# Kernel optimization log

Measured on AMD Instinct MI355X. Metric: run time of the kernel, lower is better.

The kernel has to match this reference:

```python
import jax, jax.numpy as jnp
import numpy as np

N_NODES = 100000
N_EDGES = 1600000
IN_FEATS = 64
HIDDEN = 64
N_CLASSES = 1


def setup_inputs() -> dict:
    key = jax.random.key(0)
    k0, k1, k2, k3, k4 = jax.random.split(key, 5)
    x = jax.random.normal(k0, (N_NODES, IN_FEATS), dtype=jnp.float32)
    src = jax.random.randint(k1, (N_EDGES,), 0, N_NODES, dtype=jnp.int32)
    dst = jax.random.randint(k2, (N_EDGES,), 0, N_NODES, dtype=jnp.int32)
    W1 = jax.random.normal(k3, (IN_FEATS, HIDDEN), dtype=jnp.float32) * (1.0 / np.sqrt(IN_FEATS))
    b1 = jnp.zeros((HIDDEN,), dtype=jnp.float32)
    W2 = jax.random.normal(k4, (HIDDEN, N_CLASSES), dtype=jnp.float32) * (1.0 / np.sqrt(HIDDEN))
    b2 = jnp.zeros((N_CLASSES,), dtype=jnp.float32)
    return {"x": x, "src": src, "dst": dst, "W1": W1, "b1": b1, "W2": W2, "b2": b2}


def _graph_conv(h, src, dst, W, b, n_nodes):
    # DGL GraphConv, norm='both': D_out^{-1/2} A D_in^{-1/2} h W + b
    ones = jnp.ones(src.shape[0], dtype=h.dtype)
    deg_out = jax.ops.segment_sum(ones, src, num_segments=n_nodes)
    deg_in = jax.ops.segment_sum(ones, dst, num_segments=n_nodes)
    norm_out = jnp.where(deg_out > 0, deg_out, 1.0) ** -0.5  # [N]
    norm_in = jnp.where(deg_in > 0, deg_in, 1.0) ** -0.5
    h = h * norm_out[:, None]
    # project first when it shrinks the message size (matches DGL's in>out path; math identical)
    if W.shape[1] < W.shape[0]:
        h = h @ W
    agg = jax.ops.segment_sum(h[src], dst, num_segments=n_nodes)  # [N, d]
    agg = agg * norm_in[:, None]
    if W.shape[1] >= W.shape[0]:
        agg = agg @ W
    return agg + b


def reference(x, src, dst, W1, b1, W2, b2):
    h = _graph_conv(x, src, dst, W1, b1, N_NODES)
    h = jax.nn.relu(h)
    # dropout p=0.0 -> identity
    h = _graph_conv(h, src, dst, W2, b2, N_NODES)
    return jax.nn.sigmoid(h)
```

## Files before the change

### kernel.cpp

```cpp
#include <hip/hip_runtime.h>

#define NN 100000
#define NE 1600000
#define NW 25000
#define NW4 6250
#define S  64
#define EPS (NE / S)

typedef unsigned int uint;
typedef _Float16 f16x8 __attribute__((ext_vector_type(8)));
typedef _Float16 f16x2 __attribute__((ext_vector_type(2)));
typedef float f32x4 __attribute__((ext_vector_type(4)));

__global__ void __launch_bounds__(256)
k_hist(const int* __restrict__ src, const int* __restrict__ dst,
       uint* __restrict__ partial_in, uint* __restrict__ partial_out,
       unsigned char* __restrict__ lr) {
    __shared__ uint4 cnt4[NW4];
    uint* cnt = (uint*)cnt4;
    int sl = blockIdx.x;
    int y  = blockIdx.y;
    for (int w = threadIdx.x; w < NW4; w += 256) cnt4[w] = make_uint4(0, 0, 0, 0);
    __syncthreads();
    const int* key = y ? src : dst;
    int base = sl * EPS;
    for (int i4 = threadIdx.x; i4 < EPS / 4; i4 += 256) {
        int e = base + i4 * 4;
        int4 k4 = *(const int4*)&key[e];
        uint sh0 = (uint)(k4.x & 3) * 8u, sh1 = (uint)(k4.y & 3) * 8u;
        uint sh2 = (uint)(k4.z & 3) * 8u, sh3 = (uint)(k4.w & 3) * 8u;
        uint r0 = (atomicAdd(&cnt[k4.x >> 2], 1u << sh0) >> sh0) & 0xffu;
        uint r1 = (atomicAdd(&cnt[k4.y >> 2], 1u << sh1) >> sh1) & 0xffu;
        uint r2 = (atomicAdd(&cnt[k4.z >> 2], 1u << sh2) >> sh2) & 0xffu;
        uint r3 = (atomicAdd(&cnt[k4.w >> 2], 1u << sh3) >> sh3) & 0xffu;
        if (y == 0) {
            uchar4 pk = make_uchar4((unsigned char)r0, (unsigned char)r1,
                                    (unsigned char)r2, (unsigned char)r3);
            *(uchar4*)&lr[e] = pk;
        }
    }
    __syncthreads();
    uint4* dp = (uint4*)((y ? partial_out : partial_in) + (size_t)sl * NW);
    for (int w = threadIdx.x; w < NW4; w += 256) dp[w] = cnt4[w];
}

__global__ void k_degnorm(uint* __restrict__ partial_in, const uint* __restrict__ partial_out,
                          int* __restrict__ deg_in, float* __restrict__ norm_in,
                          float* __restrict__ norm_out) {
    int w = blockIdx.x * blockDim.x + threadIdx.x;
    if (w >= NW) return;
    uint run = 0;
#pragma unroll 8
    for (int s = 0; s < S; ++s) {
        uint u = partial_in[(size_t)s * NW + w];
        partial_in[(size_t)s * NW + w] = run;
        run += u;
    }
    uint ro = 0;
#pragma unroll 8
    for (int s = 0; s < S; ++s) ro += partial_out[(size_t)s * NW + w];
    int4 dg;
    float4 fi, fo;
    {
        int d0 = run & 0xff, d1 = (run >> 8) & 0xff, d2 = (run >> 16) & 0xff, d3 = (run >> 24) & 0xff;
        dg = make_int4(d0, d1, d2, d3);
        fi.x = d0 > 0 ? rsqrtf((float)d0) : 1.0f;
        fi.y = d1 > 0 ? rsqrtf((float)d1) : 1.0f;
        fi.z = d2 > 0 ? rsqrtf((float)d2) : 1.0f;
        fi.w = d3 > 0 ? rsqrtf((float)d3) : 1.0f;
        int o0 = ro & 0xff, o1 = (ro >> 8) & 0xff, o2 = (ro >> 16) & 0xff, o3 = (ro >> 24) & 0xff;
        fo.x = o0 > 0 ? rsqrtf((float)o0) : 1.0f;
        fo.y = o1 > 0 ? rsqrtf((float)o1) : 1.0f;
        fo.z = o2 > 0 ? rsqrtf((float)o2) : 1.0f;
        fo.w = o3 > 0 ? rsqrtf((float)o3) : 1.0f;
    }
    *(int4*)&deg_in[w * 4]     = dg;
    *(float4*)&norm_in[w * 4]  = fi;
    *(float4*)&norm_out[w * 4] = fo;
}


__global__ void k_bsum(const int* __restrict__ deg_in, int* __restrict__ bsum) {
    __shared__ int red[4];
    int base = blockIdx.x * 1024;
    int s = 0;
    for (int i = threadIdx.x; i < 1024; i += 256) {
        int n = base + i;
        s += (n < NN) ? deg_in[n] : 0;
    }
#pragma unroll
    for (int off = 32; off; off >>= 1) s += __shfl_xor(s, off, 64);
    if ((threadIdx.x & 63) == 0) red[threadIdx.x >> 6] = s;
    __syncthreads();
    if (threadIdx.x == 0) bsum[blockIdx.x] = red[0] + red[1] + red[2] + red[3];
}

__global__ void k_bscan(const int* __restrict__ bsum, int* __restrict__ bofs,
                        int* __restrict__ row_ofs, int nb) {
    if (blockIdx.x == 0 && threadIdx.x == 0) {
        int run = 0;
        for (int i = 0; i < nb; ++i) { bofs[i] = run; run += bsum[i]; }
        bofs[nb] = run;
        row_ofs[NN] = run;
    }
}

__global__ void k_scan(const int* __restrict__ deg_in, const int* __restrict__ bofs,
                       int* __restrict__ row_ofs) {
    __shared__ int wofs[4];
    int t = threadIdx.x;
    int base = blockIdx.x * 1024 + t * 4;
    int d[4];
#pragma unroll
    for (int k = 0; k < 4; ++k) {
        int n = base + k;
        d[k] = (n < NN) ? deg_in[n] : 0;
    }
    int loc = d[0] + d[1] + d[2] + d[3];
    int v = loc;
    int lane = t & 63;
#pragma unroll
    for (int off = 1; off < 64; off <<= 1) {
        int u = __shfl_up(v, off, 64);
        if (lane >= off) v += u;
    }
    if (lane == 63) wofs[t >> 6] = v;
    __syncthreads();
    int w = t >> 6;
    int wbase = 0;
    if (w > 0) wbase += wofs[0];
    if (w > 1) wbase += wofs[1];
    if (w > 2) wbase += wofs[2];
    int excl = bofs[blockIdx.x] + wbase + (v - loc);
#pragma unroll
    for (int k = 0; k < 4; ++k) {
        int n = base + k;
        if (n < NN) { row_ofs[n] = excl; excl += d[k]; }
    }
}

__global__ void k_replay(const int* __restrict__ src, const int* __restrict__ dst,
                         const uint* __restrict__ base_bytes, const unsigned char* __restrict__ lr,
                         const int* __restrict__ row_ofs, int* __restrict__ csr_src) {
    int e = blockIdx.x * blockDim.x + threadIdx.x;
    if (e < NE) {
        int d  = dst[e];
        int sl = e / EPS;
        uint pw = base_bytes[(size_t)sl * NW + (d >> 2)];
        int b = (int)((pw >> ((d & 3) * 8)) & 0xffu);
        csr_src[row_ofs[d] + b + (int)lr[e]] = src[e];
    }
}

__global__ void __launch_bounds__(256)
k_proj(const float* __restrict__ x, const float* __restrict__ norm_out,
       const float* __restrict__ W1, _Float16* __restrict__ y) {
    int lane = threadIdx.x & 63;
    int col  = lane & 15;
    int kh   = lane >> 4;
    f16x8 wf[4][2];
#pragma unroll
    for (int t = 0; t < 4; ++t)
#pragma unroll
        for (int s = 0; s < 2; ++s)
#pragma unroll
            for (int j = 0; j < 8; ++j)
                wf[t][s][j] = (_Float16)W1[(s * 32 + kh * 8 + j) * 64 + t * 16 + col];
    int tile = blockIdx.x * 4 + (threadIdx.x >> 6);
    if (tile >= NN / 16) return;
    int base = tile * 16;
    int row  = base + col;
    float no = norm_out[row];
    const float* xr = &x[(size_t)row * 64 + kh * 8];
    f16x8 af[2];
#pragma unroll
    for (int s = 0; s < 2; ++s) {
        float4 v0 = *(const float4*)&xr[s * 32];
        float4 v1 = *(const float4*)&xr[s * 32 + 4];
        af[s][0] = (_Float16)(v0.x * no); af[s][1] = (_Float16)(v0.y * no);
        af[s][2] = (_Float16)(v0.z * no); af[s][3] = (_Float16)(v0.w * no);
        af[s][4] = (_Float16)(v1.x * no); af[s][5] = (_Float16)(v1.y * no);
        af[s][6] = (_Float16)(v1.z * no); af[s][7] = (_Float16)(v1.w * no);
    }
    f32x4 acc[4];
#pragma unroll
    for (int t = 0; t < 4; ++t) acc[t] = (f32x4){0.f, 0.f, 0.f, 0.f};
#pragma unroll
    for (int t = 0; t < 4; ++t) {
        acc[t] = __builtin_amdgcn_mfma_f32_16x16x32_f16(af[0], wf[t][0], acc[t], 0, 0, 0);
        acc[t] = __builtin_amdgcn_mfma_f32_16x16x32_f16(af[1], wf[t][1], acc[t], 0, 0, 0);
    }
#pragma unroll
    for (int t = 0; t < 4; ++t)
#pragma unroll
        for (int r = 0; r < 4; ++r)
            y[(size_t)(base + kh * 4 + r) * 64 + t * 16 + col] = (_Float16)acc[t][r];
}

__device__ inline float2 up2(uint u) {
    f16x2 p = __builtin_bit_cast(f16x2, u);
    return make_float2((float)p.x, (float)p.y);
}

__global__ void __launch_bounds__(256)
k_agg1(const int* __restrict__ csr_src, const int* __restrict__ row_ofs,
       const uint* __restrict__ xb, const float* __restrict__ norm_in,
       const float* __restrict__ norm_out,
       const float* __restrict__ b1, const float* __restrict__ W2,
       float* __restrict__ z) {
    int tid = threadIdx.x;
    int lane = tid & 63, q = lane >> 4, lq = lane & 15;
    int n = blockIdx.x * 4 + (tid >> 6);
    if (n >= NN) return;
    int beg = row_ofs[n], end = row_ofs[n + 1];
    float a0 = 0, a1 = 0, a2 = 0, a3 = 0;
    int ei = beg + q;
    for (; ei + 4 < end; ei += 8) {
        int sA = csr_src[ei], sB = csr_src[ei + 4];
        uint2 uA = *(const uint2*)((const char*)xb + ((size_t)sA << 7) + (lq << 3));
        uint2 uB = *(const uint2*)((const char*)xb + ((size_t)sB << 7) + (lq << 3));
        float2 pA0 = up2(uA.x), pA1 = up2(uA.y), pB0 = up2(uB.x), pB1 = up2(uB.y);
        a0 += pA0.x + pB0.x;
        a1 += pA0.y + pB0.y;
        a2 += pA1.x + pB1.x;
        a3 += pA1.y + pB1.y;
    }
    if (ei < end) {
        int sA = csr_src[ei];
        uint2 uA = *(const uint2*)((const char*)xb + ((size_t)sA << 7) + (lq << 3));
        float2 pA0 = up2(uA.x), pA1 = up2(uA.y);
        a0 += pA0.x; a1 += pA0.y; a2 += pA1.x; a3 += pA1.y;
    }
    a0 += __shfl_xor(a0, 16, 64); a0 += __shfl_xor(a0, 32, 64);
    a1 += __shfl_xor(a1, 16, 64); a1 += __shfl_xor(a1, 32, 64);
    a2 += __shfl_xor(a2, 16, 64); a2 += __shfl_xor(a2, 32, 64);
    a3 += __shfl_xor(a3, 16, 64); a3 += __shfl_xor(a3, 32, 64);
    float4 bb = *(const float4*)&b1[lq * 4];
    float4 ww = *(const float4*)&W2[lq * 4];
    float nin = norm_in[n];
    float h0 = fmaxf(a0 * nin + bb.x, 0.0f);
    float h1 = fmaxf(a1 * nin + bb.y, 0.0f);
    float h2 = fmaxf(a2 * nin + bb.z, 0.0f);
    float h3 = fmaxf(a3 * nin + bb.w, 0.0f);
    float zv = h0 * ww.x + h1 * ww.y + h2 * ww.z + h3 * ww.w;
#pragma unroll
    for (int off = 8; off; off >>= 1) zv += __shfl_xor(zv, off, 64);
    if (lane == 0) z[n] = zv * norm_out[n];
}

__global__ void k_out2(const int* __restrict__ csr_src, const int* __restrict__ row_ofs,
                       const float* __restrict__ z, const float* __restrict__ norm_in,
                       const float* __restrict__ b2, float* __restrict__ out) {
    int n = blockIdx.x * blockDim.x + threadIdx.x;
    if (n < NN) {
        int beg = row_ofs[n], end = row_ofs[n + 1];
        float a = 0.0f;
        int i = beg;
        for (; i + 3 < end; i += 4) {
            float z0 = z[csr_src[i]], z1 = z[csr_src[i + 1]];
            float z2 = z[csr_src[i + 2]], z3 = z[csr_src[i + 3]];
            a += (z0 + z1) + (z2 + z3);
        }
        for (; i < end; ++i) a += z[csr_src[i]];
        float v = a * norm_in[n] + b2[0];
        out[n] = 1.0f / (1.0f + expf(-v));
    }
}


extern "C" void kernel_launch(void* const* d_in, const int* in_sizes, int n_in,
                              void* d_out, int out_size, void* d_ws, size_t ws_size,
                              hipStream_t stream) {
    const float* x   = (const float*)d_in[0];
    const int*   src = (const int*)d_in[1];
    const int*   dst = (const int*)d_in[2];
    const float* W1  = (const float*)d_in[3];
    const float* b1  = (const float*)d_in[4];
    const float* W2  = (const float*)d_in[5];
    const float* b2  = (const float*)d_in[6];
    float* out = (float*)d_out;

    uint* W0 = (uint*)d_ws;
    uint*          partial_in  = W0;
    unsigned char* lr          = (unsigned char*)(W0 + 1600000);
    uint*          partial_out = W0 + 2000000;
    uint*          xb          = W0;
    int*           csr_src     = (int*)(W0 + 3600000);
    int*           row_ofs     = (int*)(W0 + 5200000);
    int*           deg_in      = row_ofs + NN + 32;
    float*         norm_in     = (float*)(deg_in + NN);
    float*         norm_out    = norm_in + NN;
    float*         z           = norm_out + NN;
    int*           bsum        = (int*)(z + NN);
    int*           bofs        = bsum + 128;

    int nb = (NN + 1023) / 1024;

    k_hist   <<<dim3(S, 2), 256, 0, stream>>>(src, dst, partial_in, partial_out, lr);
    k_degnorm<<<(NW + 255) / 256, 256, 0, stream>>>(partial_in, partial_out,
                                                    deg_in, norm_in, norm_out);
    k_bsum   <<<nb, 256, 0, stream>>>(deg_in, bsum);
    k_bscan  <<<1, 64, 0, stream>>>(bsum, bofs, row_ofs, nb);
    k_scan   <<<nb, 256, 0, stream>>>(deg_in, bofs, row_ofs);
    k_replay <<<(NE + 255) / 256, 256, 0, stream>>>(src, dst, partial_in, lr, row_ofs, csr_src);

    k_proj   <<<(NN / 16 + 3) / 4, 256, 0, stream>>>(x, norm_out, W1, (_Float16*)xb);
    k_agg1   <<<(NN + 3) / 4, 256, 0, stream>>>(csr_src, row_ofs, xb, norm_in, norm_out,
                                                b1, W2, z);
    k_out2   <<<(NN + 255) / 256, 256, 0, stream>>>(csr_src, row_ofs, z, norm_in, b2, out);
}
```

Baseline: 142.2 us.

## Fuse block sums into degnorm, warp-parallel bscan, persistent unrolled agg1

```diff
diff --git a/kernel.cpp b/kernel.cpp
--- a/kernel.cpp
+++ b/kernel.cpp
@@ -6,6 +6,7 @@
 #define NW4 6250
 #define S  64
 #define EPS (NE / S)
+#define AGG_GRID 2048
 
 typedef unsigned int uint;
 typedef _Float16 f16x8 __attribute__((ext_vector_type(8)));
@@ -46,22 +47,23 @@
 
 __global__ void k_degnorm(uint* __restrict__ partial_in, const uint* __restrict__ partial_out,
                           int* __restrict__ deg_in, float* __restrict__ norm_in,
-                          float* __restrict__ norm_out) {
-    int w = blockIdx.x * blockDim.x + threadIdx.x;
-    if (w >= NW) return;
-    uint run = 0;
+                          float* __restrict__ norm_out, int* __restrict__ bsum) {
+    __shared__ int red[4];
+    int w = blockIdx.x * 256 + threadIdx.x;
+    int mysum = 0;
+    if (w < NW) {
+        uint run = 0;
 #pragma unroll 8
-    for (int s = 0; s < S; ++s) {
-        uint u = partial_in[(size_t)s * NW + w];
-        partial_in[(size_t)s * NW + w] = run;
-        run += u;
-    }
-    uint ro = 0;
+        for (int s = 0; s < S; ++s) {
+            uint u = partial_in[(size_t)s * NW + w];
+            partial_in[(size_t)s * NW + w] = run;
+            run += u;
+        }
+        uint ro = 0;
 #pragma unroll 8
-    for (int s = 0; s < S; ++s) ro += partial_out[(size_t)s * NW + w];
-    int4 dg;
-    float4 fi, fo;
-    {
+        for (int s = 0; s < S; ++s) ro += partial_out[(size_t)s * NW + w];
+        int4 dg;
+        float4 fi, fo;
         int d0 = run & 0xff, d1 = (run >> 8) & 0xff, d2 = (run >> 16) & 0xff, d3 = (run >> 24) & 0xff;
         dg = make_int4(d0, d1, d2, d3);
         fi.x = d0 > 0 ? rsqrtf((float)d0) : 1.0f;
@@ -73,36 +75,34 @@
         fo.y = o1 > 0 ? rsqrtf((float)o1) : 1.0f;
         fo.z = o2 > 0 ? rsqrtf((float)o2) : 1.0f;
         fo.w = o3 > 0 ? rsqrtf((float)o3) : 1.0f;
-    }
-    *(int4*)&deg_in[w * 4]     = dg;
-    *(float4*)&norm_in[w * 4]  = fi;
-    *(float4*)&norm_out[w * 4] = fo;
-}
-
-
-__global__ void k_bsum(const int* __restrict__ deg_in, int* __restrict__ bsum) {
-    __shared__ int red[4];
-    int base = blockIdx.x * 1024;
-    int s = 0;
-    for (int i = threadIdx.x; i < 1024; i += 256) {
-        int n = base + i;
-        s += (n < NN) ? deg_in[n] : 0;
-    }
-#pragma unroll
-    for (int off = 32; off; off >>= 1) s += __shfl_xor(s, off, 64);
-    if ((threadIdx.x & 63) == 0) red[threadIdx.x >> 6] = s;
+        *(int4*)&deg_in[w * 4]     = dg;
+        *(float4*)&norm_in[w * 4]  = fi;
+        *(float4*)&norm_out[w * 4] = fo;
+        mysum = d0 + d1 + d2 + d3;
+    }
+#pragma unroll
+    for (int off = 32; off; off >>= 1) mysum += __shfl_xor(mysum, off, 64);
+    if ((threadIdx.x & 63) == 0) red[threadIdx.x >> 6] = mysum;
     __syncthreads();
     if (threadIdx.x == 0) bsum[blockIdx.x] = red[0] + red[1] + red[2] + red[3];
 }
 
 __global__ void k_bscan(const int* __restrict__ bsum, int* __restrict__ bofs,
                         int* __restrict__ row_ofs, int nb) {
-    if (blockIdx.x == 0 && threadIdx.x == 0) {
-        int run = 0;
-        for (int i = 0; i < nb; ++i) { bofs[i] = run; run += bsum[i]; }
-        bofs[nb] = run;
-        row_ofs[NN] = run;
-    }
+    int lane = threadIdx.x;
+    int v0 = (lane * 2     < nb) ? bsum[lane * 2]     : 0;
+    int v1 = (lane * 2 + 1 < nb) ? bsum[lane * 2 + 1] : 0;
+    int pair = v0 + v1;
+    int pre = pair;
+#pragma unroll
+    for (int off = 1; off < 64; off <<= 1) {
+        int u = __shfl_up(pre, off, 64);
+        if (lane >= off) pre += u;
+    }
+    int base = pre - pair;
+    if (lane * 2     < nb) bofs[lane * 2]     = base;
+    if (lane * 2 + 1 < nb) bofs[lane * 2 + 1] = base + v0;
+    if (lane == 63) { bofs[nb] = pre; row_ofs[NN] = pre; }
 }
 
 __global__ void k_scan(const int* __restrict__ deg_in, const int* __restrict__ bofs,
@@ -210,42 +210,49 @@
        float* __restrict__ z) {
     int tid = threadIdx.x;
     int lane = tid & 63, q = lane >> 4, lq = lane & 15;
-    int n = blockIdx.x * 4 + (tid >> 6);
-    if (n >= NN) return;
-    int beg = row_ofs[n], end = row_ofs[n + 1];
-    float a0 = 0, a1 = 0, a2 = 0, a3 = 0;
-    int ei = beg + q;
-    for (; ei + 4 < end; ei += 8) {
-        int sA = csr_src[ei], sB = csr_src[ei + 4];
-        uint2 uA = *(const uint2*)((const char*)xb + ((size_t)sA << 7) + (lq << 3));
-        uint2 uB = *(const uint2*)((const char*)xb + ((size_t)sB << 7) + (lq << 3));
-        float2 pA0 = up2(uA.x), pA1 = up2(uA.y), pB0 = up2(uB.x), pB1 = up2(uB.y);
-        a0 += pA0.x + pB0.x;
-        a1 += pA0.y + pB0.y;
-        a2 += pA1.x + pB1.x;
-        a3 += pA1.y + pB1.y;
-    }
-    if (ei < end) {
-        int sA = csr_src[ei];
-        uint2 uA = *(const uint2*)((const char*)xb + ((size_t)sA << 7) + (lq << 3));
-        float2 pA0 = up2(uA.x), pA1 = up2(uA.y);
-        a0 += pA0.x; a1 += pA0.y; a2 += pA1.x; a3 += pA1.y;
-    }
-    a0 += __shfl_xor(a0, 16, 64); a0 += __shfl_xor(a0, 32, 64);
-    a1 += __shfl_xor(a1, 16, 64); a1 += __shfl_xor(a1, 32, 64);
-    a2 += __shfl_xor(a2, 16, 64); a2 += __shfl_xor(a2, 32, 64);
-    a3 += __shfl_xor(a3, 16, 64); a3 += __shfl_xor(a3, 32, 64);
     float4 bb = *(const float4*)&b1[lq * 4];
     float4 ww = *(const float4*)&W2[lq * 4];
-    float nin = norm_in[n];
-    float h0 = fmaxf(a0 * nin + bb.x, 0.0f);
-    float h1 = fmaxf(a1 * nin + bb.y, 0.0f);
-    float h2 = fmaxf(a2 * nin + bb.z, 0.0f);
-    float h3 = fmaxf(a3 * nin + bb.w, 0.0f);
-    float zv = h0 * ww.x + h1 * ww.y + h2 * ww.z + h3 * ww.w;
-#pragma unroll
-    for (int off = 8; off; off >>= 1) zv += __shfl_xor(zv, off, 64);
-    if (lane == 0) z[n] = zv * norm_out[n];
+    const size_t lqo = (size_t)(lq << 3);
+    for (int n = blockIdx.x * 4 + (tid >> 6); n < NN; n += AGG_GRID * 4) {
+        int beg = row_ofs[n], end = row_ofs[n + 1];
+        float a0 = 0, a1 = 0, a2 = 0, a3 = 0;
+        int ei = beg + q;
+        for (; ei + 12 < end; ei += 16) {
+            int s0 = csr_src[ei], s1 = csr_src[ei + 4];
+            int s2 = csr_src[ei + 8], s3 = csr_src[ei + 12];
+            uint2 u0 = *(const uint2*)((const char*)xb + ((size_t)s0 << 7) + lqo);
+            uint2 u1 = *(const uint2*)((const char*)xb + ((size_t)s1 << 7) + lqo);
+            uint2 u2 = *(const uint2*)((const char*)xb + ((size_t)s2 << 7) + lqo);
+            uint2 u3 = *(const uint2*)((const char*)xb + ((size_t)s3 << 7) + lqo);
+            float2 p0 = up2(u0.x), r0 = up2(u0.y);
+            float2 p1 = up2(u1.x), r1 = up2(u1.y);
+            float2 p2 = up2(u2.x), r2 = up2(u2.y);
+            float2 p3 = up2(u3.x), r3 = up2(u3.y);
+            a0 += (p0.x + p1.x) + (p2.x + p3.x);
+            a1 += (p0.y + p1.y) + (p2.y + p3.y);
+            a2 += (r0.x + r1.x) + (r2.x + r3.x);
+            a3 += (r0.y + r1.y) + (r2.y + r3.y);
+        }
+        for (; ei < end; ei += 4) {
+            int s0 = csr_src[ei];
+            uint2 u0 = *(const uint2*)((const char*)xb + ((size_t)s0 << 7) + lqo);
+            float2 p0 = up2(u0.x), r0 = up2(u0.y);
+            a0 += p0.x; a1 += p0.y; a2 += r0.x; a3 += r0.y;
+        }
+        a0 += __shfl_xor(a0, 16, 64); a0 += __shfl_xor(a0, 32, 64);
+        a1 += __shfl_xor(a1, 16, 64); a1 += __shfl_xor(a1, 32, 64);
+        a2 += __shfl_xor(a2, 16, 64); a2 += __shfl_xor(a2, 32, 64);
+        a3 += __shfl_xor(a3, 16, 64); a3 += __shfl_xor(a3, 32, 64);
+        float nin = norm_in[n];
+        float h0 = fmaxf(a0 * nin + bb.x, 0.0f);
+        float h1 = fmaxf(a1 * nin + bb.y, 0.0f);
+        float h2 = fmaxf(a2 * nin + bb.z, 0.0f);
+        float h3 = fmaxf(a3 * nin + bb.w, 0.0f);
+        float zv = h0 * ww.x + h1 * ww.y + h2 * ww.z + h3 * ww.w;
+#pragma unroll
+        for (int off = 8; off; off >>= 1) zv += __shfl_xor(zv, off, 64);
+        if (lane == 0) z[n] = zv * norm_out[n];
+    }
 }
 
 __global__ void k_out2(const int* __restrict__ csr_src, const int* __restrict__ row_ofs,
@@ -297,15 +304,14 @@
     int nb = (NN + 1023) / 1024;
 
     k_hist   <<<dim3(S, 2), 256, 0, stream>>>(src, dst, partial_in, partial_out, lr);
-    k_degnorm<<<(NW + 255) / 256, 256, 0, stream>>>(partial_in, partial_out,
-                                                    deg_in, norm_in, norm_out);
-    k_bsum   <<<nb, 256, 0, stream>>>(deg_in, bsum);
+    k_degnorm<<<nb, 256, 0, stream>>>(partial_in, partial_out, deg_in, norm_in,
+                                      norm_out, bsum);
     k_bscan  <<<1, 64, 0, stream>>>(bsum, bofs, row_ofs, nb);
     k_scan   <<<nb, 256, 0, stream>>>(deg_in, bofs, row_ofs);
     k_replay <<<(NE + 255) / 256, 256, 0, stream>>>(src, dst, partial_in, lr, row_ofs, csr_src);
 
     k_proj   <<<(NN / 16 + 3) / 4, 256, 0, stream>>>(x, norm_out, W1, (_Float16*)xb);
-    k_agg1   <<<(NN + 3) / 4, 256, 0, stream>>>(csr_src, row_ofs, xb, norm_in, norm_out,
-                                                b1, W2, z);
+    k_agg1   <<<AGG_GRID, 256, 0, stream>>>(csr_src, row_ofs, xb, norm_in, norm_out,
+                                            b1, W2, z);
     k_out2   <<<(NN + 255) / 256, 256, 0, stream>>>(csr_src, row_ofs, z, norm_in, b2, out);
 }
```

Measured after the change: 133.2 us. 1.07x faster.
